# Optimization experiments

Hardware: AMD Instinct MI355X
Metric: run time of the kernel (lower is better)

Reference implementation:

```python
import jax, jax.numpy as jnp
import numpy as np

D = 256   # input_size
H = 512   # hidden_size
A = 4     # alpha_dim
K = 2 * A * A  # output values per input dim (binary=False -> 2 params)


def _masks():
    # MADE sequential-ordering masks, per DART.create_masks
    in_deg = np.arange(D)
    hid_deg = np.arange(H) % (D - 1)
    out_deg = np.arange(D) - 1  # arange(D) % D - 1
    m0 = (hid_deg[:, None] >= in_deg[None, :]).astype(np.float32)   # [H, D]
    mh = (hid_deg[:, None] >= hid_deg[None, :]).astype(np.float32)  # [H, H]
    ml = (out_deg[:, None] >= hid_deg[None, :]).astype(np.float32)  # [D, H]
    # repeat(1, K).view(-1, H): each output-dim row repeated K consecutive times
    ml = np.repeat(ml, K, axis=0)                                    # [D*K, H]
    return jnp.asarray(m0), jnp.asarray(mh), jnp.asarray(ml)


def setup_inputs() -> dict:
    key = jax.random.key(0)
    ks = jax.random.split(key, 10)
    B = 1024
    x = jax.random.normal(ks[0], (B, D), dtype=jnp.float32)
    def lin(k, out_dim, in_dim):
        s = 1.0 / np.sqrt(in_dim)
        kw, kb = jax.random.split(k)
        W = jax.random.uniform(kw, (out_dim, in_dim), jnp.float32, -s, s)
        b = jax.random.uniform(kb, (out_dim,), jnp.float32, -s, s)
        return W, b
    W0, b0 = lin(ks[1], H, D)
    W1, b1 = lin(ks[2], H, H)
    W2, b2 = lin(ks[3], H, H)
    Wout, bout = lin(ks[4], D * K, H)
    # unnormalized_log_p_alpha initialized to log(1/A)
    ulpa = jnp.full((1, D - 1, 1, A), -np.log(A), dtype=jnp.float32)
    return {"x": x, "W0": W0, "b0": b0, "W1": W1, "b1": b1,
            "W2": W2, "b2": b2, "Wout": Wout, "bout": bout, "ulpa": ulpa}


def reference(x, W0, b0, W1, b1, W2, b2, Wout, bout, ulpa):
    m0, mh, ml = _masks()
    B = x.shape[0]
    # masked MLP (MADE)
    h = jax.nn.relu(x @ (m0 * W0).T + b0)
    h = jax.nn.relu(h @ (mh * W1).T + b1)
    h = jax.nn.relu(h @ (mh * W2).T + b2)
    theta = (h @ (ml * Wout).T + bout).reshape(B, D, 2, A, A)
    mu = theta[:, :, 0]                      # [B, D, A, A]
    std = jnp.exp(theta[:, :, 1]) + 0.01     # [B, D, A, A]
    xe = x[:, :, None, None]
    # Normal log-prob
    log_px = -0.5 * jnp.square((xe - mu) / std) - jnp.log(std) - 0.5 * jnp.log(2.0 * jnp.pi)
    # normalized log p(alpha): [1, D-1, 1, A]
    lpa = jax.nn.log_softmax(ulpa, axis=-1)
    joint = log_px[:, :-1] + lpa             # [B, D-1, A, A]
    first = joint[:, 0, 0:1]                 # [B, 1, A]
    inner = jnp.swapaxes(joint[:, 1:], 0, 1)  # [D-2, B, A, A]
    # HMM-style forward recursion: stable log-domain chain matmul via scan
    def step(carry, m):
        # carry: [B, 1, A]; m: [B, A, A]
        new = jax.nn.logsumexp(carry[:, :, :, None] + m[:, None, :, :], axis=-2)
        return new, None
    carry, _ = jax.lax.scan(step, first, inner)
    last = log_px[:, -1, :, 0:1]             # [B, A, 1]
    log_p = jax.nn.logsumexp(carry[:, :, :, None] + last[:, None, :, :], axis=-2)  # [B,1,1]
    return log_p, theta
```

## Files before the change

### kernel.cpp

```cpp
#include <hip/hip_runtime.h>
#include <math.h>

#define Bsz 1024
#define Dd  256
#define Hh  512
#define NOUT 8192

typedef __attribute__((ext_vector_type(8))) short bf8_t;
typedef __attribute__((ext_vector_type(4))) float f4_t;

__device__ inline ushort f2b(float f) {
  union { float f; unsigned u; } c; c.f = f;
  unsigned r = c.u + 0x7fffu + ((c.u >> 16) & 1u);
  return (ushort)(r >> 16);
}

__device__ inline void async16(const ushort* g, ushort* l) {
  __builtin_amdgcn_global_load_lds((const __attribute__((address_space(1))) void*)g,
                                   (__attribute__((address_space(3))) void*)l, 16, 0, 0);
}

__device__ inline int mod255(int v) {
  if (v >= 510) return v - 510;
  if (v >= 255) return v - 255;
  return v;
}

__global__ __launch_bounds__(256) void prep(
    const float* __restrict__ x,  const float* __restrict__ W0,
    const float* __restrict__ W1, const float* __restrict__ W2,
    const float* __restrict__ Wout, const float* __restrict__ ulpa,
    ushort* __restrict__ xb, ushort* __restrict__ w0b, ushort* __restrict__ w1b,
    ushort* __restrict__ w2b, ushort* __restrict__ woutb,
    float* __restrict__ lpa, unsigned* __restrict__ bar)
{
  const int blk = blockIdx.x, tid = threadIdx.x;
  if (blk == 2496) {
    if (tid < 16) bar[tid] = 0u;
    if (tid < Dd - 1) {
      float v0 = ulpa[tid * 4 + 0], v1 = ulpa[tid * 4 + 1];
      float v2 = ulpa[tid * 4 + 2], v3 = ulpa[tid * 4 + 3];
      float m = fmaxf(fmaxf(v0, v1), fmaxf(v2, v3));
      float s = __expf(v0 - m) + __expf(v1 - m) + __expf(v2 - m) + __expf(v3 - m);
      float l = m + __logf(s);
      lpa[tid * 4 + 0] = v0 - l;
      lpa[tid * 4 + 1] = v1 - l;
      lpa[tid * 4 + 2] = v2 - l;
      lpa[tid * 4 + 3] = v3 - l;
    }
    return;
  }
  const float* src; ushort* dst; int lb, mode;
  if (blk < 128)      { src = x;    dst = xb;    lb = blk;       mode = 0; }
  else if (blk < 192) { src = W0;   dst = w0b;   lb = blk - 128; mode = 1; }
  else if (blk < 320) { src = W1;   dst = w1b;   lb = blk - 192; mode = 2; }
  else if (blk < 448) { src = W2;   dst = w2b;   lb = blk - 320; mode = 2; }
  else                { src = Wout; dst = woutb; lb = blk - 448; mode = 3; }

  const int e = lb * 2048 + tid * 8;
  float4 v0 = *(const float4*)(src + e);
  float4 v1 = *(const float4*)(src + e + 4);
  float vv[8] = {v0.x, v0.y, v0.z, v0.w, v1.x, v1.y, v1.z, v1.w};
  ushort u[8];
  if (mode == 0) {
#pragma unroll
    for (int i = 0; i < 8; i++) u[i] = f2b(vv[i]);
  } else if (mode == 1) {
    int n = e >> 8, k0 = e & 255, nd = mod255(n);
#pragma unroll
    for (int i = 0; i < 8; i++) u[i] = (nd >= k0 + i) ? f2b(vv[i]) : (ushort)0;
  } else if (mode == 2) {
    int n = e >> 9, k0 = e & 511, nd = mod255(n);
#pragma unroll
    for (int i = 0; i < 8; i++) u[i] = (nd >= mod255(k0 + i)) ? f2b(vv[i]) : (ushort)0;
  } else {
    int n = e >> 9, k0 = e & 511, nd = (n >> 5) - 1;
#pragma unroll
    for (int i = 0; i < 8; i++) u[i] = (nd >= mod255(k0 + i)) ? f2b(vv[i]) : (ushort)0;
  }
  *(ushort4*)(dst + e)     = *(ushort4*)&u[0];
  *(ushort4*)(dst + e + 4) = *(ushort4*)&u[4];
}

__device__ inline void gridbar(unsigned* bar, unsigned target) {
  __syncthreads();
  if (threadIdx.x == 0) {
    __threadfence();
    __hip_atomic_fetch_add(bar, 1u, __ATOMIC_ACQ_REL, __HIP_MEMORY_SCOPE_AGENT);
    while (__hip_atomic_load(bar, __ATOMIC_ACQUIRE, __HIP_MEMORY_SCOPE_AGENT) < target) {}
  }
  __syncthreads();
  __threadfence();
}

__device__ __forceinline__ void tile_gemm64(
    const ushort* __restrict__ A, const ushort* __restrict__ W,
    const float* __restrict__ bias, ushort* __restrict__ Ch,
    int N, int Kd, int row0, int col0, ushort* As, ushort* Bs)
{
  const int tid = threadIdx.x, lane = tid & 63, wave = tid >> 6;
  const int waveM = wave >> 1, waveN = wave & 1;
  const int fm = lane & 15, qq = lane >> 4;
  const int srow = lane >> 3, qslot = lane & 7;

  f4_t acc[2][2];
#pragma unroll
  for (int i = 0; i < 2; i++)
#pragma unroll
    for (int j = 0; j < 2; j++) acc[i][j] = (f4_t){0.f, 0.f, 0.f, 0.f};

  for (int kt = 0; kt < Kd; kt += 64) {
#pragma unroll
    for (int p = 0; p < 2; p++) {
      int rb = p * 32 + wave * 8;
      int r = rb + srow;
      int q = (qslot - r) & 7;
      async16(A + (size_t)(row0 + r) * Kd + kt + q * 8, &As[rb * 64]);
    }
#pragma unroll
    for (int p = 0; p < 2; p++) {
      int rb = p * 32 + wave * 8;
      int r = rb + srow;
      int q = (qslot - r) & 7;
      async16(W + (size_t)(col0 + r) * Kd + kt + q * 8, &Bs[rb * 64]);
    }
    __syncthreads();
#pragma unroll
    for (int t = 0; t < 2; t++) {
      bf8_t af[2], bf[2];
#pragma unroll
      for (int i = 0; i < 2; i++) {
        int r = waveM * 32 + i * 16 + fm;
        int slot = ((t * 4 + qq) + r) & 7;
        af[i] = *(const bf8_t*)&As[r * 64 + slot * 8];
      }
#pragma unroll
      for (int j = 0; j < 2; j++) {
        int r = waveN * 32 + j * 16 + fm;
        int slot = ((t * 4 + qq) + r) & 7;
        bf[j] = *(const bf8_t*)&Bs[r * 64 + slot * 8];
      }
#pragma unroll
      for (int i = 0; i < 2; i++)
#pragma unroll
        for (int j = 0; j < 2; j++)
          acc[i][j] = __builtin_amdgcn_mfma_f32_16x16x32_bf16(af[i], bf[j], acc[i][j], 0, 0, 0);
    }
    __syncthreads();
  }

#pragma unroll
  for (int j = 0; j < 2; j++) {
    int col = col0 + waveN * 32 + j * 16 + fm;
    float bv = bias[col];
#pragma unroll
    for (int i = 0; i < 2; i++) {
      int rbase = row0 + waveM * 32 + i * 16 + qq * 4;
#pragma unroll
      for (int r = 0; r < 4; r++) {
        float t = fmaxf(acc[i][j][r] + bv, 0.0f);
        Ch[(size_t)(rbase + r) * N + col] = f2b(t);
      }
    }
  }
}

__global__ __launch_bounds__(256) void mlp3(
    const ushort* __restrict__ xb,
    const ushort* __restrict__ w0b, const float* __restrict__ b0,
    const ushort* __restrict__ w1b, const float* __restrict__ b1,
    const ushort* __restrict__ w2b, const float* __restrict__ b2,
    ushort* __restrict__ h0, ushort* __restrict__ h1, ushort* __restrict__ h2,
    unsigned* __restrict__ bar)
{
  __shared__ ushort As[64 * 64];
  __shared__ ushort Bs[64 * 64];
  const int row0 = (blockIdx.x >> 3) * 64;
  const int col0 = (blockIdx.x & 7) * 64;

  tile_gemm64(xb, w0b, b0, h0, Hh, Dd, row0, col0, As, Bs);
  gridbar(bar, 128);
  tile_gemm64(h0, w1b, b1, h1, Hh, Hh, row0, col0, As, Bs);
  gridbar(bar, 256);
  tile_gemm64(h1, w2b, b2, h2, Hh, Hh, row0, col0, As, Bs);
}

__global__ __launch_bounds__(256) void gemm_big(
    const ushort* __restrict__ A, const ushort* __restrict__ W,
    const float* __restrict__ bias, float* __restrict__ Cf,
    int M, int N, int Kd)
{
  __shared__ ushort As[128 * 64];
  __shared__ ushort Bs[128 * 64];
  const int tid = threadIdx.x, lane = tid & 63, wave = tid >> 6;
  const int waveM = wave >> 1, waveN = wave & 1;
  const int row0 = blockIdx.y * 128, col0 = blockIdx.x * 128;
  const int fm = lane & 15, qq = lane >> 4;
  const int srow = lane >> 3, qslot = lane & 7;

  f4_t acc[4][4];
#pragma unroll
  for (int i = 0; i < 4; i++)
#pragma unroll
    for (int j = 0; j < 4; j++) acc[i][j] = (f4_t){0.f, 0.f, 0.f, 0.f};

  for (int kt = 0; kt < Kd; kt += 64) {
#pragma unroll
    for (int p = 0; p < 4; p++) {
      int rb = p * 32 + wave * 8;
      int r = rb + srow;
      int q = (qslot - r) & 7;
      async16(A + (size_t)(row0 + r) * Kd + kt + q * 8, &As[rb * 64]);
    }
#pragma unroll
    for (int p = 0; p < 4; p++) {
      int rb = p * 32 + wave * 8;
      int r = rb + srow;
      int q = (qslot - r) & 7;
      async16(W + (size_t)(col0 + r) * Kd + kt + q * 8, &Bs[rb * 64]);
    }
    __syncthreads();
#pragma unroll
    for (int t = 0; t < 2; t++) {
      bf8_t af[4], bf[4];
#pragma unroll
      for (int i = 0; i < 4; i++) {
        int r = waveM * 64 + i * 16 + fm;
        int slot = ((t * 4 + qq) + r) & 7;
        af[i] = *(const bf8_t*)&As[r * 64 + slot * 8];
      }
#pragma unroll
      for (int j = 0; j < 4; j++) {
        int r = waveN * 64 + j * 16 + fm;
        int slot = ((t * 4 + qq) + r) & 7;
        bf[j] = *(const bf8_t*)&Bs[r * 64 + slot * 8];
      }
#pragma unroll
      for (int i = 0; i < 4; i++)
#pragma unroll
        for (int j = 0; j < 4; j++)
          acc[i][j] = __builtin_amdgcn_mfma_f32_16x16x32_bf16(af[i], bf[j], acc[i][j], 0, 0, 0);
    }
    __syncthreads();
  }

#pragma unroll
  for (int j = 0; j < 4; j++) {
    int col = col0 + waveN * 64 + j * 16 + fm;
    float bv = bias[col];
#pragma unroll
    for (int i = 0; i < 4; i++) {
      int rbase = row0 + waveM * 64 + i * 16 + qq * 4;
#pragma unroll
      for (int r = 0; r < 4; r++)
        Cf[(size_t)(rbase + r) * N + col] = acc[i][j][r] + bv;
    }
  }
}

__global__ __launch_bounds__(256) void chain2(
    const float* __restrict__ x, const float* __restrict__ theta,
    const float* __restrict__ lpa, float* __restrict__ logp)
{
  const int b = blockIdx.x;
  const int tid = threadIdx.x;
  const int seg = tid >> 4, e = tid & 15;
  const int i = e >> 2, jj = e & 3;
  const int base = (tid & 63) & ~15;
  const float C0 = 0.91893853320467274178f;
  const float* th = theta + (size_t)b * NOUT;
  const float* xb = x + (size_t)b * Dd;
  __shared__ float Ts[16][16];

  const int d0 = 1 + seg * 16;
  const int d1 = min(d0 + 16, Dd - 1);

  auto stepm = [&](int d) -> float {
    float mu = th[d * 32 + e];
    float ls = th[d * 32 + 16 + e];
    float s  = __expf(ls) + 0.01f;
    float z  = (xb[d] - mu) * __builtin_amdgcn_rcpf(s);
    return -0.5f * z * z - __logf(s) - C0 + lpa[d * 4 + jj];
  };

  float T = stepm(d0);
  for (int d = d0 + 1; d < d1; d++) {
    float m_ = stepm(d);
    float v0 = __shfl(T, base + i * 4 + 0) + __shfl(m_, base + 0 * 4 + jj);
    float v1 = __shfl(T, base + i * 4 + 1) + __shfl(m_, base + 1 * 4 + jj);
    float v2 = __shfl(T, base + i * 4 + 2) + __shfl(m_, base + 2 * 4 + jj);
    float v3 = __shfl(T, base + i * 4 + 3) + __shfl(m_, base + 3 * 4 + jj);
    float mx = fmaxf(fmaxf(v0, v1), fmaxf(v2, v3));
    float s  = __expf(v0 - mx) + __expf(v1 - mx) + __expf(v2 - mx) + __expf(v3 - mx);
    T = mx + __logf(s);
  }
  Ts[seg][e] = T;
  __syncthreads();

  if (tid < 4) {
    const int j = tid;
    float mu = th[j], ls = th[16 + j];
    float s = __expf(ls) + 0.01f;
    float z = (xb[0] - mu) * __builtin_amdgcn_rcpf(s);
    float carry = -0.5f * z * z - __logf(s) - C0 + lpa[j];
#pragma unroll 1
    for (int sg = 0; sg < 16; sg++) {
      float c0 = __shfl(carry, 0);
      float c1 = __shfl(carry, 1);
      float c2 = __shfl(carry, 2);
      float c3 = __shfl(carry, 3);
      float v0 = c0 + Ts[sg][0 * 4 + j];
      float v1 = c1 + Ts[sg][1 * 4 + j];
      float v2 = c2 + Ts[sg][2 * 4 + j];
      float v3 = c3 + Ts[sg][3 * 4 + j];
      float mx = fmaxf(fmaxf(v0, v1), fmaxf(v2, v3));
      float ss = __expf(v0 - mx) + __expf(v1 - mx) + __expf(v2 - mx) + __expf(v3 - mx);
      carry = mx + __logf(ss);
    }
    float mu2 = th[255 * 32 + j * 4], ls2 = th[255 * 32 + 16 + j * 4];
    float s2 = __expf(ls2) + 0.01f;
    float z2 = (xb[255] - mu2) * __builtin_amdgcn_rcpf(s2);
    float v = carry - 0.5f * z2 * z2 - __logf(s2) - C0;
    float mx = fmaxf(v, __shfl_xor(v, 1));
    mx = fmaxf(mx, __shfl_xor(mx, 2));
    float ee = __expf(v - mx);
    ee += __shfl_xor(ee, 1);
    ee += __shfl_xor(ee, 2);
    if (j == 0) logp[b] = mx + __logf(ee);
  }
}

extern "C" void kernel_launch(void* const* d_in, const int* in_sizes, int n_in,
                              void* d_out, int out_size, void* d_ws, size_t ws_size,
                              hipStream_t stream)
{
  const float* x    = (const float*)d_in[0];
  const float* W0   = (const float*)d_in[1];
  const float* b0   = (const float*)d_in[2];
  const float* W1   = (const float*)d_in[3];
  const float* b1   = (const float*)d_in[4];
  const float* W2   = (const float*)d_in[5];
  const float* b2   = (const float*)d_in[6];
  const float* Wout = (const float*)d_in[7];
  const float* bout = (const float*)d_in[8];
  const float* ulpa = (const float*)d_in[9];

  float* out   = (float*)d_out;
  float* logp  = out;
  float* theta = out + Bsz;

  ushort* ws    = (ushort*)d_ws;
  ushort* xb    = ws;
  ushort* w0b   = xb + 262144;
  ushort* w1b   = w0b + 131072;
  ushort* w2b   = w1b + 262144;
  ushort* woutb = w2b + 262144;
  ushort* h0    = woutb + 4194304;
  ushort* h1    = h0 + 524288;
  ushort* h2    = h1 + 524288;
  float*  lpa   = (float*)(h2 + 524288);
  unsigned* bar = (unsigned*)(lpa + 1024);

  prep<<<2497, 256, 0, stream>>>(x, W0, W1, W2, Wout, ulpa,
                                 xb, w0b, w1b, w2b, woutb, lpa, bar);
  mlp3<<<128, 256, 0, stream>>>(xb, w0b, b0, w1b, b1, w2b, b2, h0, h1, h2, bar);
  gemm_big<<<dim3(NOUT / 128, Bsz / 128), 256, 0, stream>>>(h2, woutb, bout, theta, Bsz, NOUT, Hh);
  chain2<<<Bsz, 256, 0, stream>>>(x, theta, lpa, logp);
}
```

Before: 166.5 us.

## Replace persistent grid-barrier MLP kernel with three separate smaller-tile GEMM launches

The single persistent kernel that ran the three hidden-layer GEMMs on 128 blocks and synchronised them with atomic grid barriers is split into three launches of a templated GEMM. Each launch uses 64x32 tiles on 256 blocks, so twice as many CUs are busy and there is no spin-wait barrier. In exchange it adds two kernel launch boundaries and more redundant loads of the A operand across column tiles.

```diff
diff --git a/kernel.cpp b/kernel.cpp
--- a/kernel.cpp
+++ b/kernel.cpp
@@ -32,11 +32,10 @@
     const float* __restrict__ Wout, const float* __restrict__ ulpa,
     ushort* __restrict__ xb, ushort* __restrict__ w0b, ushort* __restrict__ w1b,
     ushort* __restrict__ w2b, ushort* __restrict__ woutb,
-    float* __restrict__ lpa, unsigned* __restrict__ bar)
+    float* __restrict__ lpa)
 {
   const int blk = blockIdx.x, tid = threadIdx.x;
   if (blk == 2496) {
-    if (tid < 16) bar[tid] = 0u;
     if (tid < Dd - 1) {
       float v0 = ulpa[tid * 4 + 0], v1 = ulpa[tid * 4 + 1];
       float v2 = ulpa[tid * 4 + 2], v3 = ulpa[tid * 4 + 3];
@@ -82,107 +81,64 @@
   *(ushort4*)(dst + e + 4) = *(ushort4*)&u[4];
 }
 
-__device__ inline void gridbar(unsigned* bar, unsigned target) {
-  __syncthreads();
-  if (threadIdx.x == 0) {
-    __threadfence();
-    __hip_atomic_fetch_add(bar, 1u, __ATOMIC_ACQ_REL, __HIP_MEMORY_SCOPE_AGENT);
-    while (__hip_atomic_load(bar, __ATOMIC_ACQUIRE, __HIP_MEMORY_SCOPE_AGENT) < target) {}
-  }
-  __syncthreads();
-  __threadfence();
-}
-
-__device__ __forceinline__ void tile_gemm64(
+template<int KD>
+__global__ __launch_bounds__(256) void gemm_s(
     const ushort* __restrict__ A, const ushort* __restrict__ W,
-    const float* __restrict__ bias, ushort* __restrict__ Ch,
-    int N, int Kd, int row0, int col0, ushort* As, ushort* Bs)
-{
+    const float* __restrict__ bias, ushort* __restrict__ Ch)
+{
+  __shared__ ushort As[64 * 64];
+  __shared__ ushort Bs[32 * 64];
   const int tid = threadIdx.x, lane = tid & 63, wave = tid >> 6;
-  const int waveM = wave >> 1, waveN = wave & 1;
+  const int row0 = blockIdx.y * 64, col0 = blockIdx.x * 32;
   const int fm = lane & 15, qq = lane >> 4;
   const int srow = lane >> 3, qslot = lane & 7;
 
-  f4_t acc[2][2];
-#pragma unroll
-  for (int i = 0; i < 2; i++)
-#pragma unroll
-    for (int j = 0; j < 2; j++) acc[i][j] = (f4_t){0.f, 0.f, 0.f, 0.f};
-
-  for (int kt = 0; kt < Kd; kt += 64) {
-#pragma unroll
-    for (int p = 0; p < 2; p++) {
-      int rb = p * 32 + wave * 8;
+  f4_t acc[2];
+  acc[0] = (f4_t){0.f, 0.f, 0.f, 0.f};
+  acc[1] = (f4_t){0.f, 0.f, 0.f, 0.f};
+
+  for (int kt = 0; kt < KD; kt += 64) {
+#pragma unroll
+    for (int a = 0; a < 2; a++) {
+      int rb = wave * 16 + a * 8;
       int r = rb + srow;
       int q = (qslot - r) & 7;
-      async16(A + (size_t)(row0 + r) * Kd + kt + q * 8, &As[rb * 64]);
-    }
-#pragma unroll
-    for (int p = 0; p < 2; p++) {
-      int rb = p * 32 + wave * 8;
+      async16(A + (size_t)(row0 + r) * KD + kt + q * 8, &As[rb * 64]);
+    }
+    {
+      int rb = wave * 8;
       int r = rb + srow;
       int q = (qslot - r) & 7;
-      async16(W + (size_t)(col0 + r) * Kd + kt + q * 8, &Bs[rb * 64]);
+      async16(W + (size_t)(col0 + r) * KD + kt + q * 8, &Bs[rb * 64]);
     }
     __syncthreads();
 #pragma unroll
     for (int t = 0; t < 2; t++) {
-      bf8_t af[2], bf[2];
-#pragma unroll
-      for (int i = 0; i < 2; i++) {
-        int r = waveM * 32 + i * 16 + fm;
-        int slot = ((t * 4 + qq) + r) & 7;
-        af[i] = *(const bf8_t*)&As[r * 64 + slot * 8];
+      int ra = wave * 16 + fm;
+      int slota = ((t * 4 + qq) + ra) & 7;
+      bf8_t af = *(const bf8_t*)&As[ra * 64 + slota * 8];
+#pragma unroll
+      for (int j = 0; j < 2; j++) {
+        int rb = j * 16 + fm;
+        int slot = ((t * 4 + qq) + rb) & 7;
+        bf8_t bf = *(const bf8_t*)&Bs[rb * 64 + slot * 8];
+        acc[j] = __builtin_amdgcn_mfma_f32_16x16x32_bf16(af, bf, acc[j], 0, 0, 0);
       }
-#pragma unroll
-      for (int j = 0; j < 2; j++) {
-        int r = waveN * 32 + j * 16 + fm;
-        int slot = ((t * 4 + qq) + r) & 7;
-        bf[j] = *(const bf8_t*)&Bs[r * 64 + slot * 8];
-      }
-#pragma unroll
-      for (int i = 0; i < 2; i++)
-#pragma unroll
-        for (int j = 0; j < 2; j++)
-          acc[i][j] = __builtin_amdgcn_mfma_f32_16x16x32_bf16(af[i], bf[j], acc[i][j], 0, 0, 0);
     }
     __syncthreads();
   }
 
 #pragma unroll
   for (int j = 0; j < 2; j++) {
-    int col = col0 + waveN * 32 + j * 16 + fm;
+    int col = col0 + j * 16 + fm;
     float bv = bias[col];
-#pragma unroll
-    for (int i = 0; i < 2; i++) {
-      int rbase = row0 + waveM * 32 + i * 16 + qq * 4;
-#pragma unroll
-      for (int r = 0; r < 4; r++) {
-        float t = fmaxf(acc[i][j][r] + bv, 0.0f);
-        Ch[(size_t)(rbase + r) * N + col] = f2b(t);
-      }
-    }
-  }
-}
-
-__global__ __launch_bounds__(256) void mlp3(
-    const ushort* __restrict__ xb,
-    const ushort* __restrict__ w0b, const float* __restrict__ b0,
-    const ushort* __restrict__ w1b, const float* __restrict__ b1,
-    const ushort* __restrict__ w2b, const float* __restrict__ b2,
-    ushort* __restrict__ h0, ushort* __restrict__ h1, ushort* __restrict__ h2,
-    unsigned* __restrict__ bar)
-{
-  __shared__ ushort As[64 * 64];
-  __shared__ ushort Bs[64 * 64];
-  const int row0 = (blockIdx.x >> 3) * 64;
-  const int col0 = (blockIdx.x & 7) * 64;
-
-  tile_gemm64(xb, w0b, b0, h0, Hh, Dd, row0, col0, As, Bs);
-  gridbar(bar, 128);
-  tile_gemm64(h0, w1b, b1, h1, Hh, Hh, row0, col0, As, Bs);
-  gridbar(bar, 256);
-  tile_gemm64(h1, w2b, b2, h2, Hh, Hh, row0, col0, As, Bs);
+    int rbase = row0 + wave * 16 + qq * 4;
+#pragma unroll
+    for (int r = 0; r < 4; r++) {
+      float t = fmaxf(acc[j][r] + bv, 0.0f);
+      Ch[(size_t)(rbase + r) * Hh + col] = f2b(t);
+    }
+  }
 }
 
 __global__ __launch_bounds__(256) void gemm_big(
@@ -359,11 +315,12 @@
   ushort* h1    = h0 + 524288;
   ushort* h2    = h1 + 524288;
   float*  lpa   = (float*)(h2 + 524288);
-  unsigned* bar = (unsigned*)(lpa + 1024);
 
   prep<<<2497, 256, 0, stream>>>(x, W0, W1, W2, Wout, ulpa,
-                                 xb, w0b, w1b, w2b, woutb, lpa, bar);
-  mlp3<<<128, 256, 0, stream>>>(xb, w0b, b0, w1b, b1, w2b, b2, h0, h1, h2, bar);
+                                 xb, w0b, w1b, w2b, woutb, lpa);
+  gemm_s<Dd><<<dim3(16, 16), 256, 0, stream>>>(xb, w0b, b0, h0);
+  gemm_s<Hh><<<dim3(16, 16), 256, 0, stream>>>(h0, w1b, b1, h1);
+  gemm_s<Hh><<<dim3(16, 16), 256, 0, stream>>>(h1, w2b, b2, h2);
   gemm_big<<<dim3(NOUT / 128, Bsz / 128), 256, 0, stream>>>(h2, woutb, bout, theta, Bsz, NOUT, Hh);
   chain2<<<Bsz, 256, 0, stream>>>(x, theta, lpa, logp);
 }
```

Measured after the change: 138.0 us. 1.21x faster.
